# Optimization experiments

Measured on AMD Instinct MI355X. Metric: run time of the kernel, lower is better.

## Reference

```python
import jax, jax.numpy as jnp
import numpy as np
from jax import lax

B = 4096        # batch
D = 13          # state dim (13th component is constant context)
STEPS = 16      # output time points
SUBSTEPS = 2    # fixed dopri5 steps per output interval

# Dormand-Prince 5(4) tableau (5th-order solution row)
A21 = 1/5
A31, A32 = 3/40, 9/40
A41, A42, A43 = 44/45, -56/15, 32/9
A51, A52, A53, A54 = 19372/6561, -25360/2187, 64448/6561, -212/729
A61, A62, A63, A64, A65 = 9017/3168, -355/33, 46732/5247, 49/176, -5103/18656
B1, B3, B4, B5, B6 = 35/384, 500/1113, 125/192, -2187/6784, 11/84


def setup_inputs() -> dict:
    key = jax.random.key(0)
    ks = jax.random.split(key, 9)
    def lin(k, fin, fout):
        return jax.random.normal(k, (fin, fout), jnp.float32) / np.float32(np.sqrt(fin))
    return {
        "y0": jax.random.normal(ks[0], (B, D), jnp.float32),
        "t_span": jnp.arange(STEPS, dtype=jnp.float32) * 0.0625,  # total horizon 1.0
        "W1": lin(ks[1], 13, 256), "b1": jnp.zeros((256,), jnp.float32),
        "W2": lin(ks[2], 256, 256), "b2": jnp.zeros((256,), jnp.float32),
        "W3": lin(ks[3], 256, 128), "b3": jnp.zeros((128,), jnp.float32),
        "W4": lin(ks[4], 128, 12) * 0.1, "b4": jnp.zeros((12,), jnp.float32),
    }


def reference(y0, t_span, W1, b1, W2, b2, W3, b3, W4, b4):
    def f(y):  # learned derivative; 13th (context) component has zero derivative
        h = jax.nn.silu(y @ W1 + b1)
        h = jax.nn.silu(h @ W2 + b2)
        h = jax.nn.silu(h @ W3 + b3)
        d = h @ W4 + b4  # [B, 12]
        return jnp.concatenate([d, jnp.zeros_like(d[..., :1])], axis=-1)  # [B, 13]

    def rk_step(y, h):
        k1 = f(y)
        k2 = f(y + h * (A21 * k1))
        k3 = f(y + h * (A31 * k1 + A32 * k2))
        k4 = f(y + h * (A41 * k1 + A42 * k2 + A43 * k3))
        k5 = f(y + h * (A51 * k1 + A52 * k2 + A53 * k3 + A54 * k4))
        k6 = f(y + h * (A61 * k1 + A62 * k2 + A63 * k3 + A64 * k4 + A65 * k5))
        return y + h * (B1 * k1 + B3 * k3 + B4 * k4 + B5 * k5 + B6 * k6)

    # fixed step sizes: SUBSTEPS dopri5 steps per output interval
    hs = jnp.repeat(jnp.diff(t_span) / SUBSTEPS, SUBSTEPS)  # [(STEPS-1)*SUBSTEPS]

    def body(y, h):
        y = rk_step(y, h)
        return y, y

    _, ys = lax.scan(body, y0, hs)
    pred_y = jnp.concatenate([y0[None], ys[SUBSTEPS - 1::SUBSTEPS]], axis=0)  # [STEPS, B, 13]
    return pred_y
```

## Files before the change

kernel.cpp:

```cpp
#include <hip/hip_runtime.h>

typedef _Float16 f16;
typedef __attribute__((ext_vector_type(8))) _Float16 f16x8;
typedef __attribute__((ext_vector_type(4))) float f32x4;

#define MFMA16(a, b, c) __builtin_amdgcn_mfma_f32_16x16x32_f16((a), (b), (c), 0, 0, 0)

__device__ __forceinline__ float silu_f(float x) {
    return x * __builtin_amdgcn_rcpf(1.f + __expf(-x));
}

__device__ __forceinline__ void pack4(f16* dst, float x0, float x1, float x2, float x3) {
    union { f16 h[4]; uint2 u; } p;
    p.h[0] = (f16)x0; p.h[1] = (f16)x1; p.h[2] = (f16)x2; p.h[3] = (f16)x3;
    *(uint2*)dst = p.u;
}

__global__ __launch_bounds__(512, 2) void ode_main(
        const float* __restrict__ y0, const float* __restrict__ tspan,
        const float* __restrict__ W1, const float* __restrict__ b1,
        const float* __restrict__ W2, const float* __restrict__ b2,
        const float* __restrict__ W3, const float* __restrict__ b3,
        const float* __restrict__ W4, const float* __restrict__ b4,
        float* __restrict__ out) {

    __shared__ f16 h0[16 * 40];
    __shared__ f16 h1[16 * 264];
    __shared__ f16 h2[16 * 264];
    __shared__ f16 h3[16 * 136];
    __shared__ float bias[656];
    __shared__ float tsh[16];

    const int tid = threadIdx.x;
    const int l = tid & 63, w = tid >> 6;
    const int g = l >> 4, col = l & 15;
    const int blk = blockIdx.x;

    f16x8 w1f[2], w2f[2][8], w3f[8], w4f[4];
#pragma unroll
    for (int a = 0; a < 2; ++a) {
        const int n = (2 * w + a) * 16 + col;
#pragma unroll
        for (int j = 0; j < 8; ++j) {
            const int k = g * 8 + j;
            w1f[a][j] = (k < 13) ? (f16)W1[k * 256 + n] : (f16)0.f;
        }
#pragma unroll
        for (int kt = 0; kt < 8; ++kt)
#pragma unroll
            for (int j = 0; j < 8; ++j)
                w2f[a][kt][j] = (f16)W2[(kt * 32 + g * 8 + j) * 256 + n];
    }
    {
        const int n3 = w * 16 + col;
#pragma unroll
        for (int kt = 0; kt < 8; ++kt)
#pragma unroll
            for (int j = 0; j < 8; ++j)
                w3f[kt][j] = (f16)W3[(kt * 32 + g * 8 + j) * 128 + n3];
    }
#pragma unroll
    for (int kt = 0; kt < 4; ++kt)
#pragma unroll
        for (int j = 0; j < 8; ++j)
            w4f[kt][j] = (col < 12) ? (f16)W4[(kt * 32 + g * 8 + j) * 12 + col] : (f16)0.f;

    for (int i = tid; i < 656; i += 512) {
        float v = 0.f;
        if (i < 256) v = b1[i];
        else if (i < 512) v = b2[i - 256];
        else if (i < 640) v = b3[i - 512];
        else if (i < 652) v = b4[i - 640];
        bias[i] = v;
    }
    if (tid < 16) tsh[tid] = tspan[tid];
    for (int i = tid; i < 640; i += 512) h0[i] = (f16)0.f;
    __syncthreads();

    float yreg[4];
#pragma unroll
    for (int j = 0; j < 4; ++j) {
        const int c = 4 * g + j;
        yreg[j] = (c < 13) ? y0[(blk * 16 + col) * 13 + c] : 0.f;
    }
    if (w == 0) {
#pragma unroll
        for (int j = 0; j < 4; ++j) {
            const int c = 4 * g + j;
            if (c < 13) {
                h0[col * 40 + c] = (f16)yreg[j];
                out[(size_t)(blk * 16 + col) * 13 + c] = yreg[j];
            }
        }
    }
    __syncthreads();

    static constexpr float AT[5][5] = {
        {0.2f, 0.f, 0.f, 0.f, 0.f},
        {3.f/40.f, 9.f/40.f, 0.f, 0.f, 0.f},
        {44.f/45.f, -56.f/15.f, 32.f/9.f, 0.f, 0.f},
        {19372.f/6561.f, -25360.f/2187.f, 64448.f/6561.f, -212.f/729.f, 0.f},
        {9017.f/3168.f, -355.f/33.f, 46732.f/5247.f, 49.f/176.f, -5103.f/18656.f}
    };

    float kreg[6][4];

    for (int step = 0; step < 30; ++step) {
        const float hstep = (tsh[(step >> 1) + 1] - tsh[step >> 1]) * 0.5f;
#pragma unroll
        for (int s = 0; s < 6; ++s) {
            f16x8 b0 = *(const f16x8*)&h0[col * 40 + g * 8];
            f32x4 acc[2];
#pragma unroll
            for (int a = 0; a < 2; ++a) acc[a] = (f32x4){0.f, 0.f, 0.f, 0.f};
#pragma unroll
            for (int a = 0; a < 2; ++a) acc[a] = MFMA16(w1f[a], b0, acc[a]);
#pragma unroll
            for (int a = 0; a < 2; ++a) {
                const int nt = 2 * w + a;
                float4 bb = *(const float4*)&bias[nt * 16 + g * 4];
                pack4(&h1[col * 264 + nt * 16 + g * 4],
                      silu_f(acc[a][0] + bb.x), silu_f(acc[a][1] + bb.y),
                      silu_f(acc[a][2] + bb.z), silu_f(acc[a][3] + bb.w));
            }
            __syncthreads();
            f16x8 hf[8];
#pragma unroll
            for (int kt = 0; kt < 8; ++kt) hf[kt] = *(const f16x8*)&h1[col * 264 + kt * 32 + g * 8];
#pragma unroll
            for (int a = 0; a < 2; ++a) acc[a] = (f32x4){0.f, 0.f, 0.f, 0.f};
#pragma unroll
            for (int kt = 0; kt < 8; ++kt)
#pragma unroll
                for (int a = 0; a < 2; ++a) acc[a] = MFMA16(w2f[a][kt], hf[kt], acc[a]);
#pragma unroll
            for (int a = 0; a < 2; ++a) {
                const int nt = 2 * w + a;
                float4 bb = *(const float4*)&bias[256 + nt * 16 + g * 4];
                pack4(&h2[col * 264 + nt * 16 + g * 4],
                      silu_f(acc[a][0] + bb.x), silu_f(acc[a][1] + bb.y),
                      silu_f(acc[a][2] + bb.z), silu_f(acc[a][3] + bb.w));
            }
            __syncthreads();
#pragma unroll
            for (int kt = 0; kt < 8; ++kt) hf[kt] = *(const f16x8*)&h2[col * 264 + kt * 32 + g * 8];
            f32x4 a3 = (f32x4){0.f, 0.f, 0.f, 0.f};
#pragma unroll
            for (int kt = 0; kt < 8; ++kt) a3 = MFMA16(w3f[kt], hf[kt], a3);
            {
                float4 bb = *(const float4*)&bias[512 + w * 16 + g * 4];
                pack4(&h3[col * 136 + w * 16 + g * 4],
                      silu_f(a3[0] + bb.x), silu_f(a3[1] + bb.y),
                      silu_f(a3[2] + bb.z), silu_f(a3[3] + bb.w));
            }
            __syncthreads();
            if (w == 0) {
                f16x8 h3f[4];
#pragma unroll
                for (int kt = 0; kt < 4; ++kt) h3f[kt] = *(const f16x8*)&h3[col * 136 + kt * 32 + g * 8];
                f32x4 a4 = (f32x4){0.f, 0.f, 0.f, 0.f};
#pragma unroll
                for (int kt = 0; kt < 4; ++kt) a4 = MFMA16(w4f[kt], h3f[kt], a4);
                float4 bb = *(const float4*)&bias[640 + g * 4];
                kreg[s][0] = a4[0] + bb.x; kreg[s][1] = a4[1] + bb.y;
                kreg[s][2] = a4[2] + bb.z; kreg[s][3] = a4[3] + bb.w;
                float x[4];
                if (s < 5) {
#pragma unroll
                    for (int j = 0; j < 4; ++j) {
                        float a2 = 0.f;
#pragma unroll
                        for (int i = 0; i <= s; ++i) a2 += AT[s][i] * kreg[i][j];
                        x[j] = yreg[j] + hstep * a2;
                    }
                } else {
#pragma unroll
                    for (int j = 0; j < 4; ++j) {
                        float a2 = (35.f/384.f) * kreg[0][j] + (500.f/1113.f) * kreg[2][j]
                                 + (125.f/192.f) * kreg[3][j] + (-2187.f/6784.f) * kreg[4][j]
                                 + (11.f/84.f) * kreg[5][j];
                        yreg[j] += hstep * a2;
                        x[j] = yreg[j];
                    }
                }
                pack4(&h0[col * 40 + g * 4], x[0], x[1], x[2], x[3]);
                if (s == 5 && (step & 1)) {
                    const int slot = (step + 1) >> 1;
#pragma unroll
                    for (int j = 0; j < 4; ++j) {
                        const int c = 4 * g + j;
                        if (c < 13)
                            out[((size_t)slot * 4096 + blk * 16 + col) * 13 + c] = yreg[j];
                    }
                }
            }
            __syncthreads();
        }
    }
}

extern "C" void kernel_launch(void* const* d_in, const int* in_sizes, int n_in,
                              void* d_out, int out_size, void* d_ws, size_t ws_size,
                              hipStream_t stream) {
    (void)in_sizes; (void)n_in; (void)out_size; (void)d_ws; (void)ws_size;
    const float* y0 = (const float*)d_in[0];
    const float* ts = (const float*)d_in[1];
    const float* W1 = (const float*)d_in[2];
    const float* b1 = (const float*)d_in[3];
    const float* W2 = (const float*)d_in[4];
    const float* b2 = (const float*)d_in[5];
    const float* W3 = (const float*)d_in[6];
    const float* b3 = (const float*)d_in[7];
    const float* W4 = (const float*)d_in[8];
    const float* b4 = (const float*)d_in[9];
    float* out = (float*)d_out;

    hipLaunchKernelGGL(ode_main, dim3(256), dim3(512), 0, stream,
                       y0, ts, W1, b1, W2, b2, W3, b3, W4, b4, out);
}
```

Measured before the change: 350.2 us.

## Compute last layer redundantly in every wave and pass state via bpermute

Every wave now runs the final 128->12 layer and the RK stage combination itself, instead of only wave 0 doing it. The next-stage input is then built in registers with ds_bpermute instead of going through the shared h0 buffer. This drops one block-wide barrier per stage and the LDS round trip for the state vector. In exchange, the layer-4 MFMAs and RK arithmetic are duplicated across all 8 waves, and converting the state to fp16 now uses round-toward-zero packing.

```diff
diff --git a/kernel.cpp b/kernel.cpp
--- a/kernel.cpp
+++ b/kernel.cpp
@@ -14,6 +14,13 @@
     union { f16 h[4]; uint2 u; } p;
     p.h[0] = (f16)x0; p.h[1] = (f16)x1; p.h[2] = (f16)x2; p.h[3] = (f16)x3;
     *(uint2*)dst = p.u;
+}
+
+__device__ __forceinline__ int pkf16(float a, float b) {
+    typedef __attribute__((ext_vector_type(2))) __fp16 fp16x2;
+    union { fp16x2 v; int i; } u;
+    u.v = __builtin_amdgcn_cvt_pkrtz(a, b);
+    return u.i;
 }
 
 __global__ __launch_bounds__(512, 2) void ode_main(
@@ -24,7 +31,6 @@
         const float* __restrict__ W4, const float* __restrict__ b4,
         float* __restrict__ out) {
 
-    __shared__ f16 h0[16 * 40];
     __shared__ f16 h1[16 * 264];
     __shared__ f16 h2[16 * 264];
     __shared__ f16 h3[16 * 136];
@@ -35,6 +41,8 @@
     const int l = tid & 63, w = tid >> 6;
     const int g = l >> 4, col = l & 15;
     const int blk = blockIdx.x;
+    const int bp0 = (32 * g + col) * 4;
+    const int bp1 = bp0 + 64;
 
     f16x8 w1f[2], w2f[2][8], w3f[8], w4f[4];
 #pragma unroll
@@ -74,8 +82,6 @@
         bias[i] = v;
     }
     if (tid < 16) tsh[tid] = tspan[tid];
-    for (int i = tid; i < 640; i += 512) h0[i] = (f16)0.f;
-    __syncthreads();
 
     float yreg[4];
 #pragma unroll
@@ -87,10 +93,7 @@
 #pragma unroll
         for (int j = 0; j < 4; ++j) {
             const int c = 4 * g + j;
-            if (c < 13) {
-                h0[col * 40 + c] = (f16)yreg[j];
-                out[(size_t)(blk * 16 + col) * 13 + c] = yreg[j];
-            }
+            if (c < 13) out[(size_t)(blk * 16 + col) * 13 + c] = yreg[j];
         }
     }
     __syncthreads();
@@ -104,12 +107,22 @@
     };
 
     float kreg[6][4];
+    f16x8 b0;
+    {
+        int h01 = pkf16(yreg[0], yreg[1]), h23 = pkf16(yreg[2], yreg[3]);
+        int u0 = __builtin_amdgcn_ds_bpermute(bp0, h01);
+        int u1 = __builtin_amdgcn_ds_bpermute(bp0, h23);
+        int u2 = __builtin_amdgcn_ds_bpermute(bp1, h01);
+        int u3 = __builtin_amdgcn_ds_bpermute(bp1, h23);
+        if (g >= 2) { u0 = 0; u1 = 0; u2 = 0; u3 = 0; }
+        union { int i[4]; f16x8 v; } u; u.i[0]=u0; u.i[1]=u1; u.i[2]=u2; u.i[3]=u3;
+        b0 = u.v;
+    }
 
     for (int step = 0; step < 30; ++step) {
         const float hstep = (tsh[(step >> 1) + 1] - tsh[step >> 1]) * 0.5f;
 #pragma unroll
         for (int s = 0; s < 6; ++s) {
-            f16x8 b0 = *(const f16x8*)&h0[col * 40 + g * 8];
             f32x4 acc[2];
 #pragma unroll
             for (int a = 0; a < 2; ++a) acc[a] = (f32x4){0.f, 0.f, 0.f, 0.f};
@@ -154,37 +167,34 @@
                       silu_f(a3[2] + bb.z), silu_f(a3[3] + bb.w));
             }
             __syncthreads();
-            if (w == 0) {
-                f16x8 h3f[4];
-#pragma unroll
-                for (int kt = 0; kt < 4; ++kt) h3f[kt] = *(const f16x8*)&h3[col * 136 + kt * 32 + g * 8];
-                f32x4 a4 = (f32x4){0.f, 0.f, 0.f, 0.f};
-#pragma unroll
-                for (int kt = 0; kt < 4; ++kt) a4 = MFMA16(w4f[kt], h3f[kt], a4);
-                float4 bb = *(const float4*)&bias[640 + g * 4];
-                kreg[s][0] = a4[0] + bb.x; kreg[s][1] = a4[1] + bb.y;
-                kreg[s][2] = a4[2] + bb.z; kreg[s][3] = a4[3] + bb.w;
-                float x[4];
-                if (s < 5) {
-#pragma unroll
-                    for (int j = 0; j < 4; ++j) {
-                        float a2 = 0.f;
-#pragma unroll
-                        for (int i = 0; i <= s; ++i) a2 += AT[s][i] * kreg[i][j];
-                        x[j] = yreg[j] + hstep * a2;
-                    }
-                } else {
-#pragma unroll
-                    for (int j = 0; j < 4; ++j) {
-                        float a2 = (35.f/384.f) * kreg[0][j] + (500.f/1113.f) * kreg[2][j]
-                                 + (125.f/192.f) * kreg[3][j] + (-2187.f/6784.f) * kreg[4][j]
-                                 + (11.f/84.f) * kreg[5][j];
-                        yreg[j] += hstep * a2;
-                        x[j] = yreg[j];
-                    }
+            f16x8 h3f[4];
+#pragma unroll
+            for (int kt = 0; kt < 4; ++kt) h3f[kt] = *(const f16x8*)&h3[col * 136 + kt * 32 + g * 8];
+            f32x4 a4 = (f32x4){0.f, 0.f, 0.f, 0.f};
+#pragma unroll
+            for (int kt = 0; kt < 4; ++kt) a4 = MFMA16(w4f[kt], h3f[kt], a4);
+            float4 bb4 = *(const float4*)&bias[640 + g * 4];
+            kreg[s][0] = a4[0] + bb4.x; kreg[s][1] = a4[1] + bb4.y;
+            kreg[s][2] = a4[2] + bb4.z; kreg[s][3] = a4[3] + bb4.w;
+            float x[4];
+            if (s < 5) {
+#pragma unroll
+                for (int j = 0; j < 4; ++j) {
+                    float a2 = 0.f;
+#pragma unroll
+                    for (int i = 0; i <= s; ++i) a2 += AT[s][i] * kreg[i][j];
+                    x[j] = yreg[j] + hstep * a2;
                 }
-                pack4(&h0[col * 40 + g * 4], x[0], x[1], x[2], x[3]);
-                if (s == 5 && (step & 1)) {
+            } else {
+#pragma unroll
+                for (int j = 0; j < 4; ++j) {
+                    float a2 = (35.f/384.f) * kreg[0][j] + (500.f/1113.f) * kreg[2][j]
+                             + (125.f/192.f) * kreg[3][j] + (-2187.f/6784.f) * kreg[4][j]
+                             + (11.f/84.f) * kreg[5][j];
+                    yreg[j] += hstep * a2;
+                    x[j] = yreg[j];
+                }
+                if ((step & 1) && w == 0) {
                     const int slot = (step + 1) >> 1;
 #pragma unroll
                     for (int j = 0; j < 4; ++j) {
@@ -194,7 +204,16 @@
                     }
                 }
             }
-            __syncthreads();
+            {
+                int h01 = pkf16(x[0], x[1]), h23 = pkf16(x[2], x[3]);
+                int u0 = __builtin_amdgcn_ds_bpermute(bp0, h01);
+                int u1 = __builtin_amdgcn_ds_bpermute(bp0, h23);
+                int u2 = __builtin_amdgcn_ds_bpermute(bp1, h01);
+                int u3 = __builtin_amdgcn_ds_bpermute(bp1, h23);
+                if (g >= 2) { u0 = 0; u1 = 0; u2 = 0; u3 = 0; }
+                union { int i[4]; f16x8 v; } u; u.i[0]=u0; u.i[1]=u1; u.i[2]=u2; u.i[3]=u3;
+                b0 = u.v;
+            }
         }
     }
 }
```

After: 361.9 us. 3.3% more time.
